# Optimization experiments

Measured on AMD Instinct MI355X. Metric: run time of the kernel, lower is better.

## Reference

```python
import jax, jax.numpy as jnp
import numpy as np

N_NODES = 100000
D_FEAT = 128
N_GATHER = 1600000
N_MACRO = 50000


def setup_inputs() -> dict:
    key = jax.random.key(0)
    k1, k2, k3 = jax.random.split(key, 3)
    node_feature = jax.random.normal(k1, (N_NODES, D_FEAT), dtype=jnp.float32)
    batch_node_ids = jax.random.randint(k2, (N_GATHER,), 0, N_NODES, dtype=jnp.int64 if jax.config.jax_enable_x64 else jnp.int32)
    batch_macro_node_ids = jnp.sort(jax.random.randint(k3, (N_GATHER,), 0, N_MACRO, dtype=jnp.int64 if jax.config.jax_enable_x64 else jnp.int32))
    return {
        "node_feature": node_feature,
        "batch_node_ids": batch_node_ids,
        "batch_macro_node_ids": batch_macro_node_ids,
        "num_macro_nodes": N_MACRO,
    }


def reference(node_feature, batch_node_ids, batch_macro_node_ids, num_macro_nodes):
    # gather: [n_gather, d]
    gathered = node_feature[batch_node_ids]
    # scatter-mean by segment id -> [num_macro_nodes, d]
    sums = jax.ops.segment_sum(gathered, batch_macro_node_ids, num_segments=num_macro_nodes)
    counts = jax.ops.segment_sum(
        jnp.ones((batch_macro_node_ids.shape[0],), dtype=node_feature.dtype),
        batch_macro_node_ids, num_segments=num_macro_nodes)
    # empty segments stay 0 (matches torch_scatter 'mean' behavior)
    return sums / jnp.maximum(counts, 1.0)[:, None]
```

## Files before the change

kernel.cpp:

```cpp
#include <hip/hip_runtime.h>
#include <hip/hip_fp16.h>

#define D_FEAT 128
#define MAX_CHUNK 1024

__global__ __launch_bounds__(256)
void convert_fp16_kernel(const float4* __restrict__ src, uint2* __restrict__ dst, int n4) {
    int i = blockIdx.x * blockDim.x + threadIdx.x;
    if (i >= n4) return;
    const float4 v = src[i];
    const __half2 a = __floats2half2_rn(v.x, v.y);
    const __half2 b = __floats2half2_rn(v.z, v.w);
    uint2 o;
    o.x = *(const unsigned int*)&a;
    o.y = *(const unsigned int*)&b;
    dst[i] = o;
}

__global__ void seg_offsets_kernel(const int* __restrict__ mids, int n_gather,
                                   int num_macro, int* __restrict__ offsets) {
    int i = blockIdx.x * blockDim.x + threadIdx.x;
    if (i >= n_gather) return;
    int cur = mids[i];
    int prev = (i == 0) ? -1 : mids[i - 1];
    for (int m = prev + 1; m <= cur; ++m) offsets[m] = i;
    if (i == n_gather - 1) {
        for (int m = cur + 1; m <= num_macro; ++m) offsets[m] = n_gather;
    }
}

__device__ __forceinline__ void acc8(float4& acc, const uint2 p) {
    const float2 lo = __half22float2(*(const __half2*)&p.x);
    const float2 hi = __half22float2(*(const __half2*)&p.y);
    acc.x += lo.x; acc.y += lo.y; acc.z += hi.x; acc.w += hi.y;
}

__global__ __launch_bounds__(256)
void pool_mean_fp16_kernel(const __half* __restrict__ tab,
                           const int* __restrict__ nids,
                           const int* __restrict__ offsets,
                           float* __restrict__ out) {
    const int m    = blockIdx.x;
    const int tid  = threadIdx.x;
    const int g    = tid >> 5;
    const int c4   = (tid & 31) << 2;

    const int start = offsets[m];
    const int cnt   = offsets[m + 1] - start;

    __shared__ int   s_idx[MAX_CHUNK];
    __shared__ float red[8][D_FEAT];

    float4 acc = make_float4(0.f, 0.f, 0.f, 0.f);

    for (int base = 0; base < cnt; base += MAX_CHUNK) {
        const int chunk = min(cnt - base, MAX_CHUNK);
        for (int t = tid; t < chunk; t += 256) s_idx[t] = nids[start + base + t];
        __syncthreads();

        int r = g;
        for (; r + 24 < chunk; r += 32) {
            const int i0 = s_idx[r];
            const int i1 = s_idx[r + 8];
            const int i2 = s_idx[r + 16];
            const int i3 = s_idx[r + 24];
            const uint2 w0 = *(const uint2*)(tab + (size_t)i0 * D_FEAT + c4);
            const uint2 w1 = *(const uint2*)(tab + (size_t)i1 * D_FEAT + c4);
            const uint2 w2 = *(const uint2*)(tab + (size_t)i2 * D_FEAT + c4);
            const uint2 w3 = *(const uint2*)(tab + (size_t)i3 * D_FEAT + c4);
            acc8(acc, w0); acc8(acc, w1); acc8(acc, w2); acc8(acc, w3);
        }
        for (; r < chunk; r += 8) {
            const uint2 w = *(const uint2*)(tab + (size_t)s_idx[r] * D_FEAT + c4);
            acc8(acc, w);
        }
        __syncthreads();
    }

    red[g][c4 + 0] = acc.x;
    red[g][c4 + 1] = acc.y;
    red[g][c4 + 2] = acc.z;
    red[g][c4 + 3] = acc.w;
    __syncthreads();

    if (tid < D_FEAT) {
        float s = 0.f;
        #pragma unroll
        for (int k = 0; k < 8; ++k) s += red[k][tid];
        const float inv = (cnt > 0) ? (1.0f / (float)cnt) : 0.0f;
        out[(size_t)m * D_FEAT + tid] = s * inv;
    }
}

__global__ __launch_bounds__(256)
void pool_mean_fp32_kernel(const float* __restrict__ feat,
                           const int* __restrict__ nids,
                           const int* __restrict__ offsets,
                           float* __restrict__ out) {
    const int m    = blockIdx.x;
    const int tid  = threadIdx.x;
    const int g    = tid >> 5;
    const int c4   = (tid & 31) << 2;

    const int start = offsets[m];
    const int cnt   = offsets[m + 1] - start;

    __shared__ int   s_idx[MAX_CHUNK];
    __shared__ float red[8][D_FEAT];

    float4 acc = make_float4(0.f, 0.f, 0.f, 0.f);
    for (int base = 0; base < cnt; base += MAX_CHUNK) {
        const int chunk = min(cnt - base, MAX_CHUNK);
        for (int t = tid; t < chunk; t += 256) s_idx[t] = nids[start + base + t];
        __syncthreads();
        int r = g;
        for (; r + 24 < chunk; r += 32) {
            const float4 v0 = *(const float4*)(feat + (size_t)s_idx[r]      * D_FEAT + c4);
            const float4 v1 = *(const float4*)(feat + (size_t)s_idx[r + 8]  * D_FEAT + c4);
            const float4 v2 = *(const float4*)(feat + (size_t)s_idx[r + 16] * D_FEAT + c4);
            const float4 v3 = *(const float4*)(feat + (size_t)s_idx[r + 24] * D_FEAT + c4);
            acc.x += v0.x + v1.x + v2.x + v3.x;
            acc.y += v0.y + v1.y + v2.y + v3.y;
            acc.z += v0.z + v1.z + v2.z + v3.z;
            acc.w += v0.w + v1.w + v2.w + v3.w;
        }
        for (; r < chunk; r += 8) {
            const float4 v = *(const float4*)(feat + (size_t)s_idx[r] * D_FEAT + c4);
            acc.x += v.x; acc.y += v.y; acc.z += v.z; acc.w += v.w;
        }
        __syncthreads();
    }

    red[g][c4 + 0] = acc.x;
    red[g][c4 + 1] = acc.y;
    red[g][c4 + 2] = acc.z;
    red[g][c4 + 3] = acc.w;
    __syncthreads();

    if (tid < D_FEAT) {
        float s = 0.f;
        #pragma unroll
        for (int k = 0; k < 8; ++k) s += red[k][tid];
        const float inv = (cnt > 0) ? (1.0f / (float)cnt) : 0.0f;
        out[(size_t)m * D_FEAT + tid] = s * inv;
    }
}

extern "C" void kernel_launch(void* const* d_in, const int* in_sizes, int n_in,
                              void* d_out, int out_size, void* d_ws, size_t ws_size,
                              hipStream_t stream) {
    const float* feat = (const float*)d_in[0];
    const int*   nids = (const int*)d_in[1];
    const int*   mids = (const int*)d_in[2];
    float*       out  = (float*)d_out;

    const int n_gather  = in_sizes[1];
    const int num_macro = out_size / D_FEAT;
    const int n_nodes   = in_sizes[0] / D_FEAT;

    int* offsets = (int*)d_ws;
    const size_t off_bytes = ((size_t)(num_macro + 1) * sizeof(int) + 255) & ~(size_t)255;
    const size_t tab_bytes = (size_t)n_nodes * D_FEAT * sizeof(__half);
    const bool use_fp16 = (off_bytes + tab_bytes) <= ws_size;

    seg_offsets_kernel<<<(n_gather + 255) / 256, 256, 0, stream>>>(
        mids, n_gather, num_macro, offsets);

    if (use_fp16) {
        __half* tab = (__half*)((char*)d_ws + off_bytes);
        const int n4 = n_nodes * D_FEAT / 4;
        convert_fp16_kernel<<<(n4 + 255) / 256, 256, 0, stream>>>(
            (const float4*)feat, (uint2*)tab, n4);
        pool_mean_fp16_kernel<<<num_macro, 256, 0, stream>>>(tab, nids, offsets, out);
    } else {
        pool_mean_fp32_kernel<<<num_macro, 256, 0, stream>>>(feat, nids, offsets, out);
    }
}
```

Before: 169.4 us.

## Slice fp16 table by feature columns and pool one segment per wave

Merges the fp16 conversion and the segment-offset kernels into a single prep launch. The converted table is stored as 8 column slices of 16 halves per node. The pooling kernel now gives each block 4 segments (one per wave) for a single slice, broadcasting indices with shuffles and reducing with xor-shuffles instead of shared memory and barriers. The idea is to shrink each slice's working set so gathered rows fit better in cache, and to cut launch and sync overhead. The cost is that every index is read 8 times and each gather is only 32 bytes.

```diff
diff --git a/kernel.cpp b/kernel.cpp
--- a/kernel.cpp
+++ b/kernel.cpp
@@ -3,31 +3,6 @@
 
 #define D_FEAT 128
 #define MAX_CHUNK 1024
-
-__global__ __launch_bounds__(256)
-void convert_fp16_kernel(const float4* __restrict__ src, uint2* __restrict__ dst, int n4) {
-    int i = blockIdx.x * blockDim.x + threadIdx.x;
-    if (i >= n4) return;
-    const float4 v = src[i];
-    const __half2 a = __floats2half2_rn(v.x, v.y);
-    const __half2 b = __floats2half2_rn(v.z, v.w);
-    uint2 o;
-    o.x = *(const unsigned int*)&a;
-    o.y = *(const unsigned int*)&b;
-    dst[i] = o;
-}
-
-__global__ void seg_offsets_kernel(const int* __restrict__ mids, int n_gather,
-                                   int num_macro, int* __restrict__ offsets) {
-    int i = blockIdx.x * blockDim.x + threadIdx.x;
-    if (i >= n_gather) return;
-    int cur = mids[i];
-    int prev = (i == 0) ? -1 : mids[i - 1];
-    for (int m = prev + 1; m <= cur; ++m) offsets[m] = i;
-    if (i == n_gather - 1) {
-        for (int m = cur + 1; m <= num_macro; ++m) offsets[m] = n_gather;
-    }
-}
 
 __device__ __forceinline__ void acc8(float4& acc, const uint2 p) {
     const float2 lo = __half22float2(*(const __half2*)&p.x);
@@ -36,59 +11,85 @@
 }
 
 __global__ __launch_bounds__(256)
-void pool_mean_fp16_kernel(const __half* __restrict__ tab,
-                           const int* __restrict__ nids,
-                           const int* __restrict__ offsets,
-                           float* __restrict__ out) {
-    const int m    = blockIdx.x;
-    const int tid  = threadIdx.x;
-    const int g    = tid >> 5;
-    const int c4   = (tid & 31) << 2;
+void prep_kernel(const float* __restrict__ feat, __half* __restrict__ tab,
+                 int n4, size_t slice_elems,
+                 const int* __restrict__ mids, int n_gather,
+                 int num_macro, int* __restrict__ offsets) {
+    const int gid = blockIdx.x * blockDim.x + threadIdx.x;
+    if (gid < n4) {
+        const float4 v = ((const float4*)feat)[gid];
+        const int node = gid >> 5;
+        const int q    = gid & 31;
+        const int s    = q >> 2;
+        const int cc4  = (q & 3) << 2;
+        const __half2 a = __floats2half2_rn(v.x, v.y);
+        const __half2 b = __floats2half2_rn(v.z, v.w);
+        uint2 o;
+        o.x = *(const unsigned int*)&a;
+        o.y = *(const unsigned int*)&b;
+        *(uint2*)(tab + (size_t)s * slice_elems + (size_t)node * 16 + cc4) = o;
+    } else {
+        const int i = gid - n4;
+        if (i >= n_gather) return;
+        const int cur  = __builtin_nontemporal_load(&mids[i]);
+        const int prev = (i == 0) ? -1 : __builtin_nontemporal_load(&mids[i - 1]);
+        for (int m = prev + 1; m <= cur; ++m) offsets[m] = i;
+        if (i == n_gather - 1) {
+            for (int m = cur + 1; m <= num_macro; ++m) offsets[m] = n_gather;
+        }
+    }
+}
 
+__global__ __launch_bounds__(256)
+void pool_mean_sliced_kernel(const __half* __restrict__ tab,
+                             const int* __restrict__ nids,
+                             const int* __restrict__ offsets,
+                             float* __restrict__ out,
+                             int num_macro, size_t slice_elems) {
+    const int slice = blockIdx.x & 7;
+    const int wave  = threadIdx.x >> 6;
+    const int m     = (blockIdx.x >> 3) * 4 + wave;
+    if (m >= num_macro) return;
+
+    const int lane   = threadIdx.x & 63;
+    const int rowpos = lane >> 2;
+    const int colq   = lane & 3;
+
+    const __half* base = tab + (size_t)slice * slice_elems;
     const int start = offsets[m];
     const int cnt   = offsets[m + 1] - start;
 
-    __shared__ int   s_idx[MAX_CHUNK];
-    __shared__ float red[8][D_FEAT];
-
     float4 acc = make_float4(0.f, 0.f, 0.f, 0.f);
 
-    for (int base = 0; base < cnt; base += MAX_CHUNK) {
-        const int chunk = min(cnt - base, MAX_CHUNK);
-        for (int t = tid; t < chunk; t += 256) s_idx[t] = nids[start + base + t];
-        __syncthreads();
+    for (int b0 = 0; b0 < cnt; b0 += 64) {
+        const int rem = min(cnt - b0, 64);
+        const int my = __builtin_nontemporal_load(
+            &nids[start + b0 + ((lane < rem) ? lane : 0)]);
 
-        int r = g;
-        for (; r + 24 < chunk; r += 32) {
-            const int i0 = s_idx[r];
-            const int i1 = s_idx[r + 8];
-            const int i2 = s_idx[r + 16];
-            const int i3 = s_idx[r + 24];
-            const uint2 w0 = *(const uint2*)(tab + (size_t)i0 * D_FEAT + c4);
-            const uint2 w1 = *(const uint2*)(tab + (size_t)i1 * D_FEAT + c4);
-            const uint2 w2 = *(const uint2*)(tab + (size_t)i2 * D_FEAT + c4);
-            const uint2 w3 = *(const uint2*)(tab + (size_t)i3 * D_FEAT + c4);
-            acc8(acc, w0); acc8(acc, w1); acc8(acc, w2); acc8(acc, w3);
+        for (int b = 0; b < rem; b += 32) {
+            const int r0 = b + rowpos;
+            const int r1 = b + 16 + rowpos;
+            const int i0 = __shfl(my, (r0 < rem) ? r0 : 0, 64);
+            const int i1 = __shfl(my, (r1 < rem) ? r1 : 0, 64);
+            const uint2 w0 = *(const uint2*)(base + (size_t)i0 * 16 + (colq << 2));
+            const uint2 w1 = *(const uint2*)(base + (size_t)i1 * 16 + (colq << 2));
+            if (r0 < rem) acc8(acc, w0);
+            if (r1 < rem) acc8(acc, w1);
         }
-        for (; r < chunk; r += 8) {
-            const uint2 w = *(const uint2*)(tab + (size_t)s_idx[r] * D_FEAT + c4);
-            acc8(acc, w);
-        }
-        __syncthreads();
     }
 
-    red[g][c4 + 0] = acc.x;
-    red[g][c4 + 1] = acc.y;
-    red[g][c4 + 2] = acc.z;
-    red[g][c4 + 3] = acc.w;
-    __syncthreads();
+    #pragma unroll
+    for (int mask = 4; mask <= 32; mask <<= 1) {
+        acc.x += __shfl_xor(acc.x, mask, 64);
+        acc.y += __shfl_xor(acc.y, mask, 64);
+        acc.z += __shfl_xor(acc.z, mask, 64);
+        acc.w += __shfl_xor(acc.w, mask, 64);
+    }
 
-    if (tid < D_FEAT) {
-        float s = 0.f;
-        #pragma unroll
-        for (int k = 0; k < 8; ++k) s += red[k][tid];
+    if (lane < 4) {
         const float inv = (cnt > 0) ? (1.0f / (float)cnt) : 0.0f;
-        out[(size_t)m * D_FEAT + tid] = s * inv;
+        float4 r = make_float4(acc.x * inv, acc.y * inv, acc.z * inv, acc.w * inv);
+        *(float4*)(out + (size_t)m * D_FEAT + slice * 16 + (colq << 2)) = r;
     }
 }
 
@@ -159,20 +160,23 @@
     const int n_nodes   = in_sizes[0] / D_FEAT;
 
     int* offsets = (int*)d_ws;
-    const size_t off_bytes = ((size_t)(num_macro + 1) * sizeof(int) + 255) & ~(size_t)255;
-    const size_t tab_bytes = (size_t)n_nodes * D_FEAT * sizeof(__half);
-    const bool use_fp16 = (off_bytes + tab_bytes) <= ws_size;
-
-    seg_offsets_kernel<<<(n_gather + 255) / 256, 256, 0, stream>>>(
-        mids, n_gather, num_macro, offsets);
+    const size_t off_bytes    = ((size_t)(num_macro + 1) * sizeof(int) + 255) & ~(size_t)255;
+    const size_t slice_elems  = (size_t)n_nodes * 16;
+    const size_t tab_bytes    = slice_elems * 8 * sizeof(__half);
+    const bool   use_fp16     = (off_bytes + tab_bytes) <= ws_size;
 
     if (use_fp16) {
         __half* tab = (__half*)((char*)d_ws + off_bytes);
-        const int n4 = n_nodes * D_FEAT / 4;
-        convert_fp16_kernel<<<(n4 + 255) / 256, 256, 0, stream>>>(
-            (const float4*)feat, (uint2*)tab, n4);
-        pool_mean_fp16_kernel<<<num_macro, 256, 0, stream>>>(tab, nids, offsets, out);
+        const int n4 = n_nodes * (D_FEAT / 4);
+        const int total_threads = n4 + n_gather;
+        prep_kernel<<<(total_threads + 255) / 256, 256, 0, stream>>>(
+            feat, tab, n4, slice_elems, mids, n_gather, num_macro, offsets);
+        const int nblocks = ((num_macro + 3) / 4) * 8;
+        pool_mean_sliced_kernel<<<nblocks, 256, 0, stream>>>(
+            tab, nids, offsets, out, num_macro, slice_elems);
     } else {
+        prep_kernel<<<(n_gather + 255) / 256, 256, 0, stream>>>(
+            feat, (__half*)nullptr, 0, 0, mids, n_gather, num_macro, offsets);
         pool_mean_fp32_kernel<<<num_macro, 256, 0, stream>>>(feat, nids, offsets, out);
     }
 }
```

Result: slower. 236.4 us (+39.6%).
